# Kernel tuning notes

Hardware: AMD Instinct MI355X
Metric: run time of the kernel (lower is better)

Reference implementation:

```python
import jax, jax.numpy as jnp
import numpy as np

DM = 1024        # model dim
NEXPERTS = 32    # experts per set; also group size t for the token permutation
EXPERTSETS = 4
EXPERTSIZE = 32  # dff = NEXPERTS * EXPERTSETS * EXPERTSIZE = 4096
BATCH, SEQ = 4, 2048


def setup_inputs() -> dict:
    key = jax.random.key(0)
    k0, k1, k2, k3 = jax.random.split(key, 4)
    scale = 0.02
    x = jax.random.normal(k0, (BATCH, SEQ, DM), jnp.float32)
    controller = jax.random.normal(k1, (DM, NEXPERTS, EXPERTSETS), jnp.float32) * scale
    f1 = jax.random.normal(k2, (DM, NEXPERTS, EXPERTSETS, EXPERTSIZE), jnp.float32) * scale
    bias = jnp.zeros((NEXPERTS, EXPERTSETS, EXPERTSIZE), jnp.float32)
    f2 = jax.random.normal(k3, (NEXPERTS, EXPERTSETS, EXPERTSIZE, DM), jnp.float32) * scale
    return {"x": x, "controller": controller, "f1": f1, "bias": bias, "f2": f2}


def reference(x, controller, f1, bias, f2):
    B, L, d = x.shape
    t = controller.shape[1]            # nexperts == group size
    g = L // t                         # number of token groups per example
    grouped = x.reshape(B, g, t, d)    # '... (b t) d -> ... b t d'

    # controller logits: '... t d, d e s -> ... t e s'
    logits = jnp.einsum('bgtd,des->bgtes', grouped, controller)
    # deterministic tiebreak over the token axis t (dim -3)
    tie = jnp.linspace(0.0, 1e-6, t, dtype=logits.dtype).reshape(t, 1, 1)
    logits = logits + tie
    # one-hot-ish permutation: for each (e, s) slot pick the argmax token in the group
    perm = (logits == jnp.max(logits, axis=-3, keepdims=True)).astype(x.dtype)
    perm = jax.lax.stop_gradient(perm)  # torch eq() produces detached bool mask

    # einsum 1 ('... t d, d e s f, ... t e s -> ... e s f'), done in the efficient order:
    # dispatch tokens to expert slots first, then the per-expert GEMM
    dispatched = jnp.einsum('bgtd,bgtes->bgesd', grouped, perm)
    inner = jax.nn.relu(jnp.einsum('bgesd,desf->bgesf', dispatched, f1) + bias)

    # einsum 2 + unpermute
    intermediate = jnp.einsum('bgesf,esfd->bgesd', inner, f2)
    out = jnp.einsum('bgesd,bgtes->bgtd', intermediate, perm)

    return out.reshape(B, L, d)
```

## Files before the change

kernel.cpp:

```cpp
#include <hip/hip_runtime.h>
#include <hip/hip_bf16.h>

#define NGROUP 256
#define NSLOT  128
#define TG     32
#define DM     1024
#define FF     32

#define LSCALE     4096.0f
#define INV_LSCALE (1.0f / 4096.0f)

typedef unsigned int  uint;
typedef unsigned short ushort;
typedef unsigned char uchar;
typedef __attribute__((ext_vector_type(4))) float f32x4;
typedef __attribute__((ext_vector_type(8))) short bf16x8;
typedef __attribute__((ext_vector_type(8))) _Float16 f16x8;

__device__ __forceinline__ ushort f2bf(float f) {
    uint u = __float_as_uint(f);
    u += 0x7FFFu + ((u >> 16) & 1u);
    return (ushort)(u >> 16);
}
__device__ __forceinline__ uint pk2(float a, float b) {
    return (uint)f2bf(a) | ((uint)f2bf(b) << 16);
}

__device__ __forceinline__ void gload_lds16(const void* g, void* l) {
    __builtin_amdgcn_global_load_lds(
        (const __attribute__((address_space(1))) uint*)g,
        (__attribute__((address_space(3))) uint*)l, 16, 0, 0);
}

__global__ __launch_bounds__(256) void k_fused1(
    const float* __restrict__ x, const float* __restrict__ ctrl,
    const float* __restrict__ f1, const float* __restrict__ f2,
    int* __restrict__ idx, uchar* __restrict__ idx8, ushort* __restrict__ xb,
    ushort* __restrict__ f1F, ushort* __restrict__ f2T)
{
    __shared__ float smem[4 * 32 * 64];
    const int t = threadIdx.x;

    if (blockIdx.x < 512) {
        float* Lp = smem;
        const int g  = blockIdx.x >> 1;
        const int nh = blockIdx.x & 1;
        const int w = t >> 6;
        const int lane = t & 63;
        const int lrow = lane & 15;
        const int lk8 = (lane >> 4) * 8;

        const size_t xoff0 = ((size_t)g * TG + lrow) * DM + w * 256 + lk8;
        const float* xr0 = x + xoff0;
        const float* xr1 = xr0 + 16 * DM;

        f32x4 ahh[2][4], ax[2][4];
#pragma unroll
        for (int mt = 0; mt < 2; ++mt)
#pragma unroll
            for (int nt = 0; nt < 4; ++nt) {
                ahh[mt][nt] = (f32x4){0.f, 0.f, 0.f, 0.f};
                ax[mt][nt]  = (f32x4){0.f, 0.f, 0.f, 0.f};
            }

        for (int ks = 0; ks < 8; ++ks) {
            f16x8 Ah[2], Al[2];
#pragma unroll
            for (int mt = 0; mt < 2; ++mt) {
                const float* p = (mt ? xr1 : xr0) + ks * 32;
                float xe[8];
                *(float4*)&xe[0] = *(const float4*)p;
                *(float4*)&xe[4] = *(const float4*)(p + 4);
                union { f16x8 v; _Float16 e[8]; } H, L;
#pragma unroll
                for (int j = 0; j < 8; ++j) {
                    const _Float16 h = (_Float16)xe[j];
                    H.e[j] = h;
                    L.e[j] = (_Float16)((xe[j] - (float)h) * LSCALE);
                }
                Ah[mt] = H.v; Al[mt] = L.v;
                if (nh == 0) {
                    uint4 o;
                    o.x = pk2(xe[0], xe[1]); o.y = pk2(xe[2], xe[3]);
                    o.z = pk2(xe[4], xe[5]); o.w = pk2(xe[6], xe[7]);
                    *(uint4*)(xb + xoff0 + (size_t)mt * 16 * DM + ks * 32) = o;
                }
            }
            const int kslice = w * 8 + ks;
#pragma unroll
            for (int nt = 0; nt < 4; ++nt) {
                const float* cp = ctrl
                    + (size_t)(kslice * 32 + ((lane >> 4) << 3)) * NSLOT
                    + nh * 64 + nt * 16 + (lane & 15);
                union { f16x8 v; _Float16 e[8]; } BH, BL;
#pragma unroll
                for (int j = 0; j < 8; ++j) {
                    const float c = cp[(size_t)j * NSLOT];
                    const _Float16 h = (_Float16)c;
                    BH.e[j] = h;
                    BL.e[j] = (_Float16)((c - (float)h) * LSCALE);
                }
#pragma unroll
                for (int mt = 0; mt < 2; ++mt) {
                    ahh[mt][nt] = __builtin_amdgcn_mfma_f32_16x16x32_f16(Ah[mt], BH.v, ahh[mt][nt], 0, 0, 0);
                    ax[mt][nt]  = __builtin_amdgcn_mfma_f32_16x16x32_f16(Al[mt], BH.v, ax[mt][nt], 0, 0, 0);
                    ax[mt][nt]  = __builtin_amdgcn_mfma_f32_16x16x32_f16(Ah[mt], BL.v, ax[mt][nt], 0, 0, 0);
                }
            }
        }

#pragma unroll
        for (int mt = 0; mt < 2; ++mt)
#pragma unroll
            for (int nt = 0; nt < 4; ++nt)
#pragma unroll
                for (int r = 0; r < 4; ++r) {
                    const int trow = mt * 16 + (lane >> 4) * 4 + r;
                    const int nl = nt * 16 + lrow;
                    Lp[(w * TG + trow) * 64 + nl] =
                        ahh[mt][nt][r] + ax[mt][nt][r] * INV_LSCALE;
                }
        __syncthreads();

        for (int i = t * 4; i < TG * 64; i += 256 * 4) {
            f32x4 s0 = *(const f32x4*)&Lp[i];
            f32x4 s1 = *(const f32x4*)&Lp[2048 + i];
            f32x4 s2 = *(const f32x4*)&Lp[4096 + i];
            f32x4 s3 = *(const f32x4*)&Lp[6144 + i];
            *(f32x4*)&Lp[i] = (s0 + s1) + (s2 + s3);
        }
        __syncthreads();

        if (t < 64) {
            const int n = t;
            float best = -1e30f;
            int bi = 0;
#pragma unroll
            for (int tt = 0; tt < TG; ++tt) {
                const float v = Lp[tt * 64 + n] + (float)tt * (1e-6f / 31.0f);
                if (v >= best) { best = v; bi = tt; }
            }
            idx[g * NSLOT + nh * 64 + n] = bi;
            idx8[g * NSLOT + nh * 64 + n] = (uchar)bi;
        }
    } else if (blockIdx.x < 768) {
        float* Ltr = smem;
        const int i1 = blockIdx.x - 512;
        const int es = i1 >> 1;
        const int dh = i1 & 1;
        for (int d0 = dh * 512; d0 < dh * 512 + 512; d0 += 64) {
            const int dd = t >> 2, f0 = (t & 3) * 8;
            const float* src = f1 + (size_t)(d0 + dd) * 4096 + es * FF + f0;
            float4 a = *(const float4*)src;
            float4 b = *(const float4*)(src + 4);
            __syncthreads();
            float* Lq = &Ltr[dd * 33 + f0];
            Lq[0] = a.x; Lq[1] = a.y; Lq[2] = a.z; Lq[3] = a.w;
            Lq[4] = b.x; Lq[5] = b.y; Lq[6] = b.z; Lq[7] = b.w;
            __syncthreads();
            const int f = t & 31, koct = t >> 5;
            const int nt = f >> 4;
            const int kg = d0 + koct * 8;
            const int kslice = kg >> 5;
            const int lane2 = (f & 15) | (((kg >> 3) & 3) << 4);
            uint4 o;
            o.x = pk2(Ltr[(koct * 8 + 0) * 33 + f], Ltr[(koct * 8 + 1) * 33 + f]);
            o.y = pk2(Ltr[(koct * 8 + 2) * 33 + f], Ltr[(koct * 8 + 3) * 33 + f]);
            o.z = pk2(Ltr[(koct * 8 + 4) * 33 + f], Ltr[(koct * 8 + 5) * 33 + f]);
            o.w = pk2(Ltr[(koct * 8 + 6) * 33 + f], Ltr[(koct * 8 + 7) * 33 + f]);
            *(uint4*)(f1F + ((((size_t)es * 2 + nt) * 32 + kslice) * 64 + lane2) * 8) = o;
        }
    } else {
        float* Ltr = smem;
        const int i2 = blockIdx.x - 768;
        const int es = i2 >> 2;
        const int dq = i2 & 3;
        for (int d0 = dq * 256; d0 < dq * 256 + 256; d0 += 64) {
            const int f = t >> 3, ds = (t & 7) * 8;
            const float* src = f2 + (size_t)es * (FF * DM) + f * DM + d0 + ds;
            float4 a = *(const float4*)src;
            float4 b = *(const float4*)(src + 4);
            __syncthreads();
            Ltr[(ds + 0) * 33 + f] = a.x; Ltr[(ds + 1) * 33 + f] = a.y;
            Ltr[(ds + 2) * 33 + f] = a.z; Ltr[(ds + 3) * 33 + f] = a.w;
            Ltr[(ds + 4) * 33 + f] = b.x; Ltr[(ds + 5) * 33 + f] = b.y;
            Ltr[(ds + 6) * 33 + f] = b.z; Ltr[(ds + 7) * 33 + f] = b.w;
            __syncthreads();
            const int dd = t >> 2, f0 = (t & 3) * 8;
            uint4 o;
            o.x = pk2(Ltr[dd * 33 + f0 + 0], Ltr[dd * 33 + f0 + 1]);
            o.y = pk2(Ltr[dd * 33 + f0 + 2], Ltr[dd * 33 + f0 + 3]);
            o.z = pk2(Ltr[dd * 33 + f0 + 4], Ltr[dd * 33 + f0 + 5]);
            o.w = pk2(Ltr[dd * 33 + f0 + 6], Ltr[dd * 33 + f0 + 7]);
            *(uint4*)(f2T + (size_t)es * (FF * DM) + (d0 + dd) * FF + f0) = o;
        }
    }
}

__global__ __launch_bounds__(256) void k_h_mfma(
    const ushort* __restrict__ xb, const ushort* __restrict__ f1F,
    const float* __restrict__ bias, const int* __restrict__ idx,
    ushort* __restrict__ Hb)
{
    const int es = blockIdx.x >> 2;
    const int gq = blockIdx.x & 3;
    const int w = threadIdx.x >> 6;
    const int lane = threadIdx.x & 63;
    const int lrow = lane & 15;
    const int lk8 = (lane >> 4) * 8;

    const int ga = gq * 64 + w * 16 + lrow;
    const int tok = idx[ga * NSLOT + es];
    const ushort* abase = xb + ((size_t)ga * TG + tok) * DM + lk8;
    const ushort* bbase = f1F + (size_t)es * 2 * 32 * 512 + (size_t)lane * 8;

    f32x4 acc[2] = {(f32x4){0.f, 0.f, 0.f, 0.f}, (f32x4){0.f, 0.f, 0.f, 0.f}};

#pragma unroll 4
    for (int kslice = 0; kslice < 32; ++kslice) {
        const bf16x8 A = *(const bf16x8*)(abase + kslice * 32);
#pragma unroll
        for (int nt = 0; nt < 2; ++nt) {
            const bf16x8 B = *(const bf16x8*)(bbase + ((size_t)nt * 32 + kslice) * 512);
            acc[nt] = __builtin_amdgcn_mfma_f32_16x16x32_bf16(A, B, acc[nt], 0, 0, 0);
        }
    }

#pragma unroll
    for (int nt = 0; nt < 2; ++nt) {
        const int f = nt * 16 + lrow;
        const float bv = bias[es * FF + f];
#pragma unroll
        for (int r = 0; r < 4; ++r) {
            const int g = gq * 64 + w * 16 + (lane >> 4) * 4 + r;
            const float hv = fmaxf(acc[nt][r] + bv, 0.0f);
            Hb[(size_t)g * (NSLOT * FF) + es * FF + f] = f2bf(hv);
        }
    }
}

__global__ __launch_bounds__(256) void k_out_mfma(
    const ushort* __restrict__ Hb, const ushort* __restrict__ f2T,
    const uchar* __restrict__ idx8, float* __restrict__ out)
{
    extern __shared__ char smK3[];
    float* OL   = (float*)smK3;
    char*  Ring = smK3 + 131072;

    const int D0 = (blockIdx.x & 15) * 64;
    const int G0 = (blockIdx.x >> 4) * 16;
    const int tid = threadIdx.x;
    const int w = tid >> 6;
    const int lane = tid & 63;
    const int gl = lane & 15;
    const int sq = lane >> 4;
    const int dq = w * 4 + sq;

    for (int i = tid * 4; i < 32768; i += 1024)
        *(f32x4*)&OL[i] = (f32x4){0.f, 0.f, 0.f, 0.f};
    uint ui[32];
    {
        const uint4* p = (const uint4*)(idx8 + (size_t)(G0 + gl) * NSLOT);
#pragma unroll
        for (int k = 0; k < 8; ++k) {
            const uint4 v = p[k];
            ui[k * 4 + 0] = v.x; ui[k * 4 + 1] = v.y;
            ui[k * 4 + 2] = v.z; ui[k * 4 + 3] = v.w;
        }
    }
    __syncthreads();

    const ushort* ap  = f2T + (size_t)(D0 + w * 16 + gl) * FF + sq * 8;
    const ushort* bps = Hb + (size_t)(G0 + gl) * (NSLOT * FF) + sq * 8;
    char* ring = Ring + w * 8192;

#pragma unroll
    for (int s = 0; s < 3; ++s) {
        gload_lds16(ap  + (size_t)s * (FF * DM), ring + s * 2048);
        gload_lds16(bps + (size_t)s * FF,        ring + s * 2048 + 1024);
    }

    const int sOL = (dq << 4) | (dq ^ gl);

#pragma unroll 4
    for (int e = 0; e < 128; ++e) {
        {
            const int en = (e + 3) & 127;
            char* slot = ring + ((e + 3) & 3) * 2048;
            gload_lds16(ap  + (size_t)en * (FF * DM), slot);
            gload_lds16(bps + (size_t)en * FF,        slot + 1024);
        }
        asm volatile("s_waitcnt vmcnt(6)" ::: "memory");

        const char* slot = ring + (e & 3) * 2048;
        const bf16x8 afr = *(const bf16x8*)(slot + lane * 16);
        const bf16x8 bfr = *(const bf16x8*)(slot + 1024 + lane * 16);
        const f32x4 d = __builtin_amdgcn_mfma_f32_16x16x32_bf16(
            afr, bfr, (f32x4){0.f, 0.f, 0.f, 0.f}, 0, 0, 0);
        const uint tv = (ui[e >> 2] >> ((e & 3) * 8)) & 0xFFu;
        float* olp = &OL[tv * 1024 + sOL * 4];
        *(f32x4*)olp = *(const f32x4*)olp + d;
    }
    asm volatile("s_waitcnt vmcnt(0)" ::: "memory");
    __syncthreads();

    {
        const int g = tid >> 4, dqe = tid & 15;
        const int se = (dqe << 4) | (dqe ^ g);
#pragma unroll 4
        for (int t = 0; t < TG; ++t) {
            const f32x4 v = *(const f32x4*)&OL[t * 1024 + se * 4];
            *(f32x4*)&out[((size_t)(G0 + g) * TG + t) * DM + D0 + dqe * 4] = v;
        }
    }
}

extern "C" void kernel_launch(void* const* d_in, const int* in_sizes, int n_in,
                              void* d_out, int out_size, void* d_ws, size_t ws_size,
                              hipStream_t stream) {
    (void)in_sizes; (void)n_in; (void)out_size; (void)ws_size;
    const float* x    = (const float*)d_in[0];
    const float* ctrl = (const float*)d_in[1];
    const float* f1   = (const float*)d_in[2];
    const float* bias = (const float*)d_in[3];
    const float* f2   = (const float*)d_in[4];
    float* out = (float*)d_out;

    char* ws = (char*)d_ws;
    int*    idx  = (int*)ws;
    ushort* Hb   = (ushort*)(ws + 131072);
    ushort* f1F  = (ushort*)(ws + 2228224);
    ushort* f2T  = (ushort*)(ws + 10616832);
    ushort* xb   = (ushort*)(ws + 19005440);
    uchar*  idx8 = (uchar*)(ws + 35782656);

    k_fused1<<<1280, 256, 0, stream>>>(x, ctrl, f1, f2, idx, idx8, xb, f1F, f2T);

    k_h_mfma<<<NSLOT * 4, 256, 0, stream>>>(xb, f1F, bias, idx, Hb);

    const size_t lds3 = 163840;
    hipFuncSetAttribute((const void*)k_out_mfma,
                        hipFuncAttributeMaxDynamicSharedMemorySize, (int)lds3);
    k_out_mfma<<<256, 256, lds3, stream>>>(Hb, f2T, idx8, out);
}
```

Measured before the change: 75.20 us.

## Compute all 128 router slots per token-group block instead of splitting halves

The router-logit section now has one block per token group covering all 128 expert slots, where before two blocks each covered half. Each x tile is loaded and split into fp16 hi/lo parts once instead of twice, and the bf16 copy of x is written by every block. In exchange the block holds twice as many accumulators, which raises register pressure, and it needs 64KB of dynamic LDS, which lowers occupancy. The grid also shrinks from 1280 to 1024 blocks, so there is less parallelism for the router phase.

```diff
diff --git a/kernel.cpp b/kernel.cpp
--- a/kernel.cpp
+++ b/kernel.cpp
@@ -38,13 +38,12 @@
     int* __restrict__ idx, uchar* __restrict__ idx8, ushort* __restrict__ xb,
     ushort* __restrict__ f1F, ushort* __restrict__ f2T)
 {
-    __shared__ float smem[4 * 32 * 64];
+    extern __shared__ char fsm[];
     const int t = threadIdx.x;
 
-    if (blockIdx.x < 512) {
-        float* Lp = smem;
-        const int g  = blockIdx.x >> 1;
-        const int nh = blockIdx.x & 1;
+    if (blockIdx.x < 256) {
+        float* Lp = (float*)fsm;
+        const int g = blockIdx.x;
         const int w = t >> 6;
         const int lane = t & 63;
         const int lrow = lane & 15;
@@ -54,11 +53,11 @@
         const float* xr0 = x + xoff0;
         const float* xr1 = xr0 + 16 * DM;
 
-        f32x4 ahh[2][4], ax[2][4];
+        f32x4 ahh[2][8], ax[2][8];
 #pragma unroll
         for (int mt = 0; mt < 2; ++mt)
 #pragma unroll
-            for (int nt = 0; nt < 4; ++nt) {
+            for (int nt = 0; nt < 8; ++nt) {
                 ahh[mt][nt] = (f32x4){0.f, 0.f, 0.f, 0.f};
                 ax[mt][nt]  = (f32x4){0.f, 0.f, 0.f, 0.f};
             }
@@ -79,19 +78,17 @@
                     L.e[j] = (_Float16)((xe[j] - (float)h) * LSCALE);
                 }
                 Ah[mt] = H.v; Al[mt] = L.v;
-                if (nh == 0) {
-                    uint4 o;
-                    o.x = pk2(xe[0], xe[1]); o.y = pk2(xe[2], xe[3]);
-                    o.z = pk2(xe[4], xe[5]); o.w = pk2(xe[6], xe[7]);
-                    *(uint4*)(xb + xoff0 + (size_t)mt * 16 * DM + ks * 32) = o;
-                }
+                uint4 o;
+                o.x = pk2(xe[0], xe[1]); o.y = pk2(xe[2], xe[3]);
+                o.z = pk2(xe[4], xe[5]); o.w = pk2(xe[6], xe[7]);
+                *(uint4*)(xb + xoff0 + (size_t)mt * 16 * DM + ks * 32) = o;
             }
             const int kslice = w * 8 + ks;
 #pragma unroll
-            for (int nt = 0; nt < 4; ++nt) {
+            for (int nt = 0; nt < 8; ++nt) {
                 const float* cp = ctrl
                     + (size_t)(kslice * 32 + ((lane >> 4) << 3)) * NSLOT
-                    + nh * 64 + nt * 16 + (lane & 15);
+                    + nt * 16 + (lane & 15);
                 union { f16x8 v; _Float16 e[8]; } BH, BL;
 #pragma unroll
                 for (int j = 0; j < 8; ++j) {
@@ -112,40 +109,40 @@
 #pragma unroll
         for (int mt = 0; mt < 2; ++mt)
 #pragma unroll
-            for (int nt = 0; nt < 4; ++nt)
+            for (int nt = 0; nt < 8; ++nt)
 #pragma unroll
                 for (int r = 0; r < 4; ++r) {
                     const int trow = mt * 16 + (lane >> 4) * 4 + r;
                     const int nl = nt * 16 + lrow;
-                    Lp[(w * TG + trow) * 64 + nl] =
+                    Lp[(w * TG + trow) * NSLOT + nl] =
                         ahh[mt][nt][r] + ax[mt][nt][r] * INV_LSCALE;
                 }
         __syncthreads();
 
-        for (int i = t * 4; i < TG * 64; i += 256 * 4) {
+        for (int i = t * 4; i < TG * NSLOT; i += 256 * 4) {
             f32x4 s0 = *(const f32x4*)&Lp[i];
-            f32x4 s1 = *(const f32x4*)&Lp[2048 + i];
-            f32x4 s2 = *(const f32x4*)&Lp[4096 + i];
-            f32x4 s3 = *(const f32x4*)&Lp[6144 + i];
+            f32x4 s1 = *(const f32x4*)&Lp[4096 + i];
+            f32x4 s2 = *(const f32x4*)&Lp[8192 + i];
+            f32x4 s3 = *(const f32x4*)&Lp[12288 + i];
             *(f32x4*)&Lp[i] = (s0 + s1) + (s2 + s3);
         }
         __syncthreads();
 
-        if (t < 64) {
+        if (t < NSLOT) {
             const int n = t;
             float best = -1e30f;
             int bi = 0;
 #pragma unroll
             for (int tt = 0; tt < TG; ++tt) {
-                const float v = Lp[tt * 64 + n] + (float)tt * (1e-6f / 31.0f);
+                const float v = Lp[tt * NSLOT + n] + (float)tt * (1e-6f / 31.0f);
                 if (v >= best) { best = v; bi = tt; }
             }
-            idx[g * NSLOT + nh * 64 + n] = bi;
-            idx8[g * NSLOT + nh * 64 + n] = (uchar)bi;
-        }
-    } else if (blockIdx.x < 768) {
-        float* Ltr = smem;
-        const int i1 = blockIdx.x - 512;
+            idx[g * NSLOT + n] = bi;
+            idx8[g * NSLOT + n] = (uchar)bi;
+        }
+    } else if (blockIdx.x < 512) {
+        float* Ltr = (float*)fsm;
+        const int i1 = blockIdx.x - 256;
         const int es = i1 >> 1;
         const int dh = i1 & 1;
         for (int d0 = dh * 512; d0 < dh * 512 + 512; d0 += 64) {
@@ -171,8 +168,8 @@
             *(uint4*)(f1F + ((((size_t)es * 2 + nt) * 32 + kslice) * 64 + lane2) * 8) = o;
         }
     } else {
-        float* Ltr = smem;
-        const int i2 = blockIdx.x - 768;
+        float* Ltr = (float*)fsm;
+        const int i2 = blockIdx.x - 512;
         const int es = i2 >> 2;
         const int dq = i2 & 3;
         for (int d0 = dq * 256; d0 < dq * 256 + 256; d0 += 64) {
@@ -334,7 +331,10 @@
     ushort* xb   = (ushort*)(ws + 19005440);
     uchar*  idx8 = (uchar*)(ws + 35782656);
 
-    k_fused1<<<1280, 256, 0, stream>>>(x, ctrl, f1, f2, idx, idx8, xb, f1F, f2T);
+    const size_t lds1 = 65536;
+    hipFuncSetAttribute((const void*)k_fused1,
+                        hipFuncAttributeMaxDynamicSharedMemorySize, (int)lds1);
+    k_fused1<<<1024, 256, lds1, stream>>>(x, ctrl, f1, f2, idx, idx8, xb, f1F, f2T);
 
     k_h_mfma<<<NSLOT * 4, 256, 0, stream>>>(xb, f1F, bias, idx, Hb);
 
```

Measured after the change: 120.3 us. 1.6x slower.
